# Kernel tuning notes

Hardware: AMD Instinct MI355X
Metric: run time of the kernel (lower is better)

Reference implementation:

```python
import jax, jax.numpy as jnp
import numpy as np

NEURONS = 4096
K = 512

def setup_inputs() -> dict:
    key = jax.random.key(0)
    s = jax.random.normal(key, (16384, NEURONS), dtype=jnp.float32)
    return {"s": s}

def reference(s) -> jnp.ndarray:
    # Original: sort each row ascending, zero the smallest (neurons - k) entries,
    # i.e. keep only the k largest values per row. With continuous random inputs
    # (no ties) this equals thresholding at the k-th largest value per row.
    topk_vals, _ = jax.lax.top_k(s, K)          # [B, K], descending
    thresh = topk_vals[:, -1:]                   # k-th largest per row, [B, 1]
    return jnp.where(s >= thresh, s, jnp.zeros((), dtype=s.dtype))
```

## Files before the change

### kernel.cpp

```cpp
#include <hip/hip_runtime.h>

#define ROWS 16384
#define COLS 4096
#define KSEL 512
#define THREADS 256
#define NCOPY0 8
#define HSTRIDE 260

__device__ __forceinline__ unsigned map_f(float f) {
    unsigned u = __float_as_uint(f);
    return u ^ (0x80000000u | (unsigned)((int)u >> 31));
}
__device__ __forceinline__ float unmap_f(unsigned m) {
    return __uint_as_float(m ^ (0x80000000u | ~(unsigned)((int)m >> 31)));
}

__device__ __forceinline__ void select_digit(unsigned n0, unsigned n1, unsigned n2,
                                             unsigned n3, int lane, int shift,
                                             unsigned& prefix, unsigned& kk) {
    unsigned ls3 = n3, ls2 = n3 + n2, ls1 = ls2 + n1, tot = ls1 + n0;
    unsigned S = tot;
#pragma unroll
    for (int off = 1; off < 64; off <<= 1) {
        unsigned o = __shfl(S, lane + off);
        S += (lane + off < 64) ? o : 0u;
    }
    const unsigned R = S - tot;
    const unsigned S3 = R + ls3, S2 = R + ls2, S1 = R + ls1, S0 = R + tot;
    unsigned dig = 0, nk = 0;
    bool found = false;
    if (S3 >= kk && R  < kk) { dig = 4 * lane + 3; nk = kk - R;  found = true; }
    if (S2 >= kk && S3 < kk) { dig = 4 * lane + 2; nk = kk - S3; found = true; }
    if (S1 >= kk && S2 < kk) { dig = 4 * lane + 1; nk = kk - S2; found = true; }
    if (S0 >= kk && S1 < kk) { dig = 4 * lane + 0; nk = kk - S1; found = true; }
    unsigned long long m = __ballot(found);
    int src = (int)__ffsll(m) - 1;
    prefix |= (unsigned)__shfl(dig, src) << shift;
    kk = (unsigned)__shfl(nk, src);
}

__global__ __launch_bounds__(THREADS, 8) void kwta_kernel(const float* __restrict__ in,
                                                          float* __restrict__ out) {
    __shared__ __align__(16) unsigned hist[(NCOPY0 + 3) * HSTRIDE];

    const int tid  = threadIdx.x;
    const int lane = tid & 63;
    const int row  = blockIdx.x;

    const float4* __restrict__ inrow  = (const float4*)(in  + (size_t)row * COLS);
    float4*       __restrict__ outrow = (float4*)(out + (size_t)row * COLS);

    unsigned v[16];
#pragma unroll
    for (int i = 0; i < 4; i++) {
        float4 f = inrow[tid + THREADS * i];
        v[4 * i + 0] = map_f(f.x);
        v[4 * i + 1] = map_f(f.y);
        v[4 * i + 2] = map_f(f.z);
        v[4 * i + 3] = map_f(f.w);
    }

    {
        const uint4 z = make_uint4(0u, 0u, 0u, 0u);
#pragma unroll
        for (int i = 0; i < 3; i++) {
            int w4 = tid + THREADS * i;
            if (w4 < (NCOPY0 + 3) * HSTRIDE / 4) ((uint4*)hist)[w4] = z;
        }
    }
    __syncthreads();

    unsigned prefix = 0;
    unsigned kk = KSEL;

    {
        unsigned* h0 = hist + (tid & (NCOPY0 - 1)) * HSTRIDE;
#pragma unroll
        for (int i = 0; i < 16; i++) atomicAdd(&h0[v[i] >> 24], 1u);
        __syncthreads();
        unsigned n0 = 0, n1 = 0, n2 = 0, n3 = 0;
#pragma unroll
        for (int c = 0; c < NCOPY0; c++) {
            uint4 t = ((const uint4*)(hist + c * HSTRIDE))[lane];
            n0 += t.x; n1 += t.y; n2 += t.z; n3 += t.w;
        }
        select_digit(n0, n1, n2, n3, lane, 24, prefix, kk);
    }

#pragma unroll
    for (int pass = 1; pass < 4; pass++) {
        const int shift = 24 - 8 * pass;
        const int hs = shift + 8;
        unsigned* hp = hist + (NCOPY0 + pass - 1) * HSTRIDE;
#pragma unroll
        for (int i = 0; i < 16; i++) {
            if (((v[i] ^ prefix) >> hs) == 0u)
                atomicAdd(&hp[(v[i] >> shift) & 255u], 1u);
        }
        __syncthreads();
        uint4 t = ((const uint4*)hp)[lane];
        select_digit(t.x, t.y, t.z, t.w, lane, shift, prefix, kk);
    }

#pragma unroll
    for (int i = 0; i < 4; i++) {
        float4 o;
        o.x = (v[4 * i + 0] >= prefix) ? unmap_f(v[4 * i + 0]) : 0.0f;
        o.y = (v[4 * i + 1] >= prefix) ? unmap_f(v[4 * i + 1]) : 0.0f;
        o.z = (v[4 * i + 2] >= prefix) ? unmap_f(v[4 * i + 2]) : 0.0f;
        o.w = (v[4 * i + 3] >= prefix) ? unmap_f(v[4 * i + 3]) : 0.0f;
        outrow[tid + THREADS * i] = o;
    }
}

extern "C" void kernel_launch(void* const* d_in, const int* in_sizes, int n_in,
                              void* d_out, int out_size, void* d_ws, size_t ws_size,
                              hipStream_t stream) {
    const float* s = (const float*)d_in[0];
    float* out = (float*)d_out;
    kwta_kernel<<<ROWS, THREADS, 0, stream>>>(s, out);
}
```

Baseline: 426.8 us.

## Replace final radix passes with small-pool rank selection and use nontemporal IO

After the first two 8-bit radix passes, rows whose candidate bucket holds at most 64 elements gather those candidates into shared memory. One wavefront then finds the exact k-th value by rank counting, which skips two histogram passes and their barriers. Rows with a larger bucket fall back to the original remaining passes. Global loads and stores are also switched to nontemporal builtins to reduce cache pollution on this streaming kernel.

New measurement: 411.4 us. 1.04x faster.

```diff
diff --git a/kernel.cpp b/kernel.cpp
--- a/kernel.cpp
+++ b/kernel.cpp
@@ -6,6 +6,10 @@
 #define THREADS 256
 #define NCOPY0 8
 #define HSTRIDE 260
+#define HWORDS ((NCOPY0 + 3) * HSTRIDE)
+
+typedef float    f32x4 __attribute__((ext_vector_type(4)));
+typedef unsigned u32x4 __attribute__((ext_vector_type(4)));
 
 __device__ __forceinline__ unsigned map_f(float f) {
     unsigned u = __float_as_uint(f);
@@ -17,7 +21,8 @@
 
 __device__ __forceinline__ void select_digit(unsigned n0, unsigned n1, unsigned n2,
                                              unsigned n3, int lane, int shift,
-                                             unsigned& prefix, unsigned& kk) {
+                                             unsigned& prefix, unsigned& kk,
+                                             unsigned& cnt) {
     unsigned ls3 = n3, ls2 = n3 + n2, ls1 = ls2 + n1, tot = ls1 + n0;
     unsigned S = tot;
 #pragma unroll
@@ -27,33 +32,34 @@
     }
     const unsigned R = S - tot;
     const unsigned S3 = R + ls3, S2 = R + ls2, S1 = R + ls1, S0 = R + tot;
-    unsigned dig = 0, nk = 0;
+    unsigned dig = 0, nk = 0, cn = 0;
     bool found = false;
-    if (S3 >= kk && R  < kk) { dig = 4 * lane + 3; nk = kk - R;  found = true; }
-    if (S2 >= kk && S3 < kk) { dig = 4 * lane + 2; nk = kk - S3; found = true; }
-    if (S1 >= kk && S2 < kk) { dig = 4 * lane + 1; nk = kk - S2; found = true; }
-    if (S0 >= kk && S1 < kk) { dig = 4 * lane + 0; nk = kk - S1; found = true; }
+    if (S3 >= kk && R  < kk) { dig = 4 * lane + 3; nk = kk - R;  cn = n3; found = true; }
+    if (S2 >= kk && S3 < kk) { dig = 4 * lane + 2; nk = kk - S3; cn = n2; found = true; }
+    if (S1 >= kk && S2 < kk) { dig = 4 * lane + 1; nk = kk - S2; cn = n1; found = true; }
+    if (S0 >= kk && S1 < kk) { dig = 4 * lane + 0; nk = kk - S1; cn = n0; found = true; }
     unsigned long long m = __ballot(found);
     int src = (int)__ffsll(m) - 1;
     prefix |= (unsigned)__shfl(dig, src) << shift;
-    kk = (unsigned)__shfl(nk, src);
+    kk  = (unsigned)__shfl(nk, src);
+    cnt = (unsigned)__shfl(cn, src);
 }
 
 __global__ __launch_bounds__(THREADS, 8) void kwta_kernel(const float* __restrict__ in,
                                                           float* __restrict__ out) {
-    __shared__ __align__(16) unsigned hist[(NCOPY0 + 3) * HSTRIDE];
+    __shared__ __align__(16) unsigned hist[HWORDS];
 
     const int tid  = threadIdx.x;
     const int lane = tid & 63;
     const int row  = blockIdx.x;
 
-    const float4* __restrict__ inrow  = (const float4*)(in  + (size_t)row * COLS);
-    float4*       __restrict__ outrow = (float4*)(out + (size_t)row * COLS);
+    const f32x4* __restrict__ inrow  = (const f32x4*)(in  + (size_t)row * COLS);
+    f32x4*       __restrict__ outrow = (f32x4*)(out + (size_t)row * COLS);
 
     unsigned v[16];
 #pragma unroll
     for (int i = 0; i < 4; i++) {
-        float4 f = inrow[tid + THREADS * i];
+        f32x4 f = __builtin_nontemporal_load(inrow + tid + THREADS * i);
         v[4 * i + 0] = map_f(f.x);
         v[4 * i + 1] = map_f(f.y);
         v[4 * i + 2] = map_f(f.z);
@@ -61,17 +67,18 @@
     }
 
     {
-        const uint4 z = make_uint4(0u, 0u, 0u, 0u);
+        const u32x4 z = {0u, 0u, 0u, 0u};
 #pragma unroll
         for (int i = 0; i < 3; i++) {
             int w4 = tid + THREADS * i;
-            if (w4 < (NCOPY0 + 3) * HSTRIDE / 4) ((uint4*)hist)[w4] = z;
+            if (w4 < HWORDS / 4) ((u32x4*)hist)[w4] = z;
         }
     }
     __syncthreads();
 
     unsigned prefix = 0;
     unsigned kk = KSEL;
+    unsigned cnt = 0;
 
     {
         unsigned* h0 = hist + (tid & (NCOPY0 - 1)) * HSTRIDE;
@@ -81,35 +88,73 @@
         unsigned n0 = 0, n1 = 0, n2 = 0, n3 = 0;
 #pragma unroll
         for (int c = 0; c < NCOPY0; c++) {
-            uint4 t = ((const uint4*)(hist + c * HSTRIDE))[lane];
+            u32x4 t = ((const u32x4*)(hist + c * HSTRIDE))[lane];
             n0 += t.x; n1 += t.y; n2 += t.z; n3 += t.w;
         }
-        select_digit(n0, n1, n2, n3, lane, 24, prefix, kk);
+        select_digit(n0, n1, n2, n3, lane, 24, prefix, kk, cnt);
     }
 
-#pragma unroll
-    for (int pass = 1; pass < 4; pass++) {
-        const int shift = 24 - 8 * pass;
-        const int hs = shift + 8;
-        unsigned* hp = hist + (NCOPY0 + pass - 1) * HSTRIDE;
+    {
+        unsigned* hp = hist + NCOPY0 * HSTRIDE;
 #pragma unroll
         for (int i = 0; i < 16; i++) {
-            if (((v[i] ^ prefix) >> hs) == 0u)
-                atomicAdd(&hp[(v[i] >> shift) & 255u], 1u);
+            if (((v[i] ^ prefix) >> 24) == 0u)
+                atomicAdd(&hp[(v[i] >> 16) & 255u], 1u);
         }
         __syncthreads();
-        uint4 t = ((const uint4*)hp)[lane];
-        select_digit(t.x, t.y, t.z, t.w, lane, shift, prefix, kk);
+        u32x4 t = ((const u32x4*)hp)[lane];
+        select_digit(t.x, t.y, t.z, t.w, lane, 16, prefix, kk, cnt);
+    }
+
+    unsigned thresh;
+    if (cnt <= 64u) {
+        unsigned* pool   = hist + (NCOPY0 + 1) * HSTRIDE;
+        unsigned* pcount = pool + 64;
+#pragma unroll
+        for (int i = 0; i < 16; i++) {
+            if (((v[i] ^ prefix) >> 16) == 0u) {
+                unsigned slot = atomicAdd(pcount, 1u);
+                pool[slot] = v[i];
+            }
+        }
+        __syncthreads();
+        unsigned x = (lane < (int)cnt) ? pool[lane] : 0u;
+        unsigned g = 0, e = 0;
+        for (unsigned j = 0; j < cnt; j++) {
+            unsigned y = pool[j];
+            g += (y > x) ? 1u : 0u;
+            e += (y == x) ? 1u : 0u;
+        }
+        bool found = (lane < (int)cnt) && (g < kk) && (g + e >= kk);
+        unsigned long long m = __ballot(found);
+        int src = (int)__ffsll(m) - 1;
+        thresh = (unsigned)__shfl(x, src);
+    } else {
+#pragma unroll
+        for (int pass = 2; pass < 4; pass++) {
+            const int shift = 24 - 8 * pass;
+            const int hs = shift + 8;
+            unsigned* hp = hist + (NCOPY0 + pass - 1) * HSTRIDE;
+#pragma unroll
+            for (int i = 0; i < 16; i++) {
+                if (((v[i] ^ prefix) >> hs) == 0u)
+                    atomicAdd(&hp[(v[i] >> shift) & 255u], 1u);
+            }
+            __syncthreads();
+            u32x4 t = ((const u32x4*)hp)[lane];
+            select_digit(t.x, t.y, t.z, t.w, lane, shift, prefix, kk, cnt);
+        }
+        thresh = prefix;
     }
 
 #pragma unroll
     for (int i = 0; i < 4; i++) {
-        float4 o;
-        o.x = (v[4 * i + 0] >= prefix) ? unmap_f(v[4 * i + 0]) : 0.0f;
-        o.y = (v[4 * i + 1] >= prefix) ? unmap_f(v[4 * i + 1]) : 0.0f;
-        o.z = (v[4 * i + 2] >= prefix) ? unmap_f(v[4 * i + 2]) : 0.0f;
-        o.w = (v[4 * i + 3] >= prefix) ? unmap_f(v[4 * i + 3]) : 0.0f;
-        outrow[tid + THREADS * i] = o;
+        f32x4 o;
+        o.x = (v[4 * i + 0] >= thresh) ? unmap_f(v[4 * i + 0]) : 0.0f;
+        o.y = (v[4 * i + 1] >= thresh) ? unmap_f(v[4 * i + 1]) : 0.0f;
+        o.z = (v[4 * i + 2] >= thresh) ? unmap_f(v[4 * i + 2]) : 0.0f;
+        o.w = (v[4 * i + 3] >= thresh) ? unmap_f(v[4 * i + 3]) : 0.0f;
+        __builtin_nontemporal_store(o, outrow + tid + THREADS * i);
     }
 }
 
```
